# Performance work log

Hardware: AMD Instinct MI355X
Metric: run time of the kernel (lower is better)

## Reference

```python
import jax, jax.numpy as jnp
import numpy as np

K = 3            # TAGConv default number of hops
NUM_GRAPHS = 128 # graphs in the batch (for global_add_pool)


def _gcn_norm(src, dst, n):
    # PyG gcn_norm (symmetric, no self-loops): w_e = d[src]^-1/2 * d[dst]^-1/2
    deg = jnp.zeros((n,), jnp.float32).at[dst].add(1.0)
    dinv = jnp.where(deg > 0, jax.lax.rsqrt(deg), 0.0)
    return dinv[src] * dinv[dst]


def _tagconv(x, src, dst, wn, W, b):
    # out = sum_{k=0..K} (norm_adj^k x) @ W[k] + b
    n = x.shape[0]
    h = x
    out = h @ W[0]
    for k in range(1, K + 1):
        h = jax.ops.segment_sum(h[src] * wn[:, None], dst, num_segments=n)
        out = out + h @ W[k]
    return out + b


def setup_inputs() -> dict:
    key = jax.random.key(0)
    ks = jax.random.split(key, 8)
    N, E, D, H = 50000, 800000, 64, 64
    x = jax.random.normal(ks[0], (N, D), jnp.float32)
    edge_index = jax.random.randint(ks[1], (2, E), 0, N, dtype=jnp.int32)
    batch_ids = jnp.sort(jax.random.randint(ks[2], (N,), 0, NUM_GRAPHS, dtype=jnp.int32))
    def glorot(k, sh):
        return jax.random.normal(k, sh, jnp.float32) / np.float32(np.sqrt(sh[-2]))
    W0 = glorot(ks[3], (K + 1, D, H)); b0 = jnp.zeros((H,), jnp.float32)
    W1 = glorot(ks[4], (K + 1, H, H)); b1 = jnp.zeros((H,), jnp.float32)
    alpha0 = jnp.full((1,), 0.25, jnp.float32)  # PReLU default init
    alpha1 = jnp.full((1,), 0.25, jnp.float32)
    Wout = glorot(ks[5], (H, 1)); bout = jnp.zeros((1,), jnp.float32)
    return dict(x=x, edge_index=edge_index, batch_ids=batch_ids,
                W0=W0, b0=b0, W1=W1, b1=b1,
                alpha0=alpha0, alpha1=alpha1, Wout=Wout, bout=bout)


def reference(x, edge_index, batch_ids, W0, b0, W1, b1, alpha0, alpha1, Wout, bout):
    src, dst = edge_index[0], edge_index[1]
    wn = _gcn_norm(src, dst, x.shape[0])
    # layer 0: TAGConv -> (dropout=identity in eval) -> PReLU
    h = _tagconv(x, src, dst, wn, W0, b0)
    h = jnp.where(h >= 0, h, alpha0 * h)
    # layer 1
    h = _tagconv(h, src, dst, wn, W1, b1)
    h = jnp.where(h >= 0, h, alpha1 * h)
    # global_add_pool over graphs, then linear critic head
    g = jax.ops.segment_sum(h, batch_ids, num_segments=NUM_GRAPHS)  # [G, H]
    return g @ Wout + bout  # [G, 1]
```

## Files before the change

kernel.cpp:

```cpp
#include <hip/hip_runtime.h>
#include <hip/hip_bf16.h>
#include <hip/hip_fp16.h>

#define D 64
#define GRAPHS 128

using bf16x8 = __attribute__((ext_vector_type(8))) short;
using f32x4  = __attribute__((ext_vector_type(4))) float;


__device__ __forceinline__ float bf2f(unsigned short u) {
    return __uint_as_float(((unsigned)u) << 16);
}
__device__ __forceinline__ unsigned short f2bf(float f) {
    unsigned u = __float_as_uint(f);
    unsigned r = (u + 0x7FFFu + ((u >> 16) & 1u)) >> 16;
    return (unsigned short)r;
}


__global__ void deg_prep_kernel(const int* __restrict__ dst, int* __restrict__ deg,
                                int* __restrict__ pos, int E, int EB4,
                                const float* __restrict__ W0, const float* __restrict__ W1,
                                unsigned short* __restrict__ WF0, unsigned short* __restrict__ WF1,
                                const float* __restrict__ x, unsigned short* __restrict__ H, int NH) {
    int b = blockIdx.x;
    if (b < EB4) {
        int e0 = (b * 256 + threadIdx.x) * 4;
        if (e0 + 4 <= E) {
            int4 d4 = *(const int4*)(dst + e0);
            int4 p;
            p.x = atomicAdd(&deg[d4.x], 1);
            p.y = atomicAdd(&deg[d4.y], 1);
            p.z = atomicAdd(&deg[d4.z], 1);
            p.w = atomicAdd(&deg[d4.w], 1);
            *(int4*)(pos + e0) = p;
        } else {
            for (int e = e0; e < E; ++e) pos[e] = atomicAdd(&deg[dst[e]], 1);
        }
    } else if (b < EB4 + 128) {
        int idx = (b - EB4) * 256 + threadIdx.x;
        int i = idx & 16383;
        int j = i & 7, lane = (i >> 3) & 63, ct = (i >> 9) & 3, kt = i >> 11;
        int n = ct * 16 + (lane & 15);
        int k = kt * 32 + (lane >> 4) * 8 + j;
        if (idx < 16384) WF0[i] = f2bf(W0[k * 64 + n]);
        else             WF1[i] = f2bf(W1[k * 64 + n]);
    } else {
        int i = (b - EB4 - 128) * 256 + threadIdx.x;
        if (i < NH) {
            int n = i >> 3, f = (i & 7) * 8;
            float4 x0 = *(const float4*)(x + (size_t)n * 64 + f);
            float4 x1 = *(const float4*)(x + (size_t)n * 64 + f + 4);
            bf16x8 pk;
            pk[0] = f2bf(x0.x); pk[1] = f2bf(x0.y); pk[2] = f2bf(x0.z); pk[3] = f2bf(x0.w);
            pk[4] = f2bf(x1.x); pk[5] = f2bf(x1.y); pk[6] = f2bf(x1.z); pk[7] = f2bf(x1.w);
            *(bf16x8*)(H + (size_t)n * 256 + f) = pk;
        }
    }
}


__global__ void scan_all_kernel(const int* __restrict__ deg, float* __restrict__ dinv,
                                int* __restrict__ pdeg, int* __restrict__ rowstart,
                                unsigned int* __restrict__ ep, int* __restrict__ total, int N) {
    __shared__ int s[256];
    __shared__ int base_sh;
    int i = blockIdx.x * 256 + threadIdx.x;
    int d = 0, p = 0;
    if (i < N) {
        d = deg[i];
        dinv[i] = d > 0 ? rsqrtf((float)d) : 0.0f;
        p = (d + 7) & ~7;
        pdeg[i] = p;
    }
    s[threadIdx.x] = p;
    __syncthreads();
    for (int st = 1; st < 256; st <<= 1) {
        int add = (threadIdx.x >= st) ? s[threadIdx.x - st] : 0;
        __syncthreads();
        s[threadIdx.x] += add;
        __syncthreads();
    }
    if (threadIdx.x == 255) base_sh = atomicAdd(total, s[255]);
    __syncthreads();
    if (i < N) {
        int excl = base_sh + s[threadIdx.x] - p;
        rowstart[i] = excl;
        for (int q = excl + d; q < excl + p; ++q) ep[q] = 0u;
    }
}


__global__ void scatter_kernel(const int* __restrict__ src, const int* __restrict__ dst,
                               const int* __restrict__ pos, const float* __restrict__ dinv,
                               const int* __restrict__ rowstart, unsigned int* __restrict__ ep, int E) {
    int e0 = (blockIdx.x * 256 + threadIdx.x) * 4;
    if (e0 + 4 <= E) {
        int4 s4 = *(const int4*)(src + e0);
        int4 d4 = *(const int4*)(dst + e0);
        int4 p4 = *(const int4*)(pos + e0);
        float v0 = dinv[s4.x], v1 = dinv[s4.y], v2 = dinv[s4.z], v3 = dinv[s4.w];
        int r0 = rowstart[d4.x], r1 = rowstart[d4.y], r2 = rowstart[d4.z], r3 = rowstart[d4.w];
        ep[r0 + p4.x] = (unsigned)s4.x | ((unsigned)__half_as_ushort(__float2half(v0)) << 16);
        ep[r1 + p4.y] = (unsigned)s4.y | ((unsigned)__half_as_ushort(__float2half(v1)) << 16);
        ep[r2 + p4.z] = (unsigned)s4.z | ((unsigned)__half_as_ushort(__float2half(v2)) << 16);
        ep[r3 + p4.w] = (unsigned)s4.w | ((unsigned)__half_as_ushort(__float2half(v3)) << 16);
    } else {
        for (int e = e0; e < E; ++e) {
            int dd = dst[e], ss = src[e];
            ep[rowstart[dd] + pos[e]] = (unsigned)ss | ((unsigned)__half_as_ushort(__float2half(dinv[ss])) << 16);
        }
    }
}


#define GROWS 8

__global__ __launch_bounds__(512, 8)
void gather_kernel(const unsigned short* __restrict__ in,
                   unsigned short* __restrict__ out,
                   const int* __restrict__ rowstart, const int* __restrict__ pdeg,
                   const float* __restrict__ dinv, const unsigned int* __restrict__ ep, int N) {
    int wid = blockIdx.x * GROWS + (threadIdx.x >> 6);
    if (wid >= N) return;
    int lane = threadIdx.x & 63;
    int g  = lane >> 3;
    int fl = (lane & 7) * 8;

    int start = __builtin_amdgcn_readfirstlane(rowstart[wid]);
    int cnt   = __builtin_amdgcn_readfirstlane(pdeg[wid]);
    float dd  = dinv[wid];

    float a0=0.f,a1=0.f,a2=0.f,a3=0.f,a4=0.f,a5=0.f,a6=0.f,a7=0.f;
    float c0=0.f,c1=0.f,c2=0.f,c3=0.f,c4=0.f,c5=0.f,c6=0.f,c7=0.f;
    unsigned eA = 0, eB = 0;
    if (cnt > 0) {
        eA = ep[start + g];
        eB = (8 < cnt) ? ep[start + 8 + g] : 0u;
    }
    for (int i = 0; i < cnt; i += 16) {
        unsigned cA = eA, cB = eB;
        if (i + 16 < cnt) {
            eA = ep[start + i + 16 + g];
            eB = (i + 24 < cnt) ? ep[start + i + 24 + g] : 0u;
        }
        bf16x8 rA = *(const bf16x8*)(in + (size_t)(cA & 0xFFFFu) * 256 + fl);
        bf16x8 rB = *(const bf16x8*)(in + (size_t)(cB & 0xFFFFu) * 256 + fl);
        float wA = __half2float(__ushort_as_half((unsigned short)(cA >> 16)));
        float wB = __half2float(__ushort_as_half((unsigned short)(cB >> 16)));
        a0 = fmaf(wA, bf2f((unsigned short)rA[0]), a0);
        a1 = fmaf(wA, bf2f((unsigned short)rA[1]), a1);
        a2 = fmaf(wA, bf2f((unsigned short)rA[2]), a2);
        a3 = fmaf(wA, bf2f((unsigned short)rA[3]), a3);
        a4 = fmaf(wA, bf2f((unsigned short)rA[4]), a4);
        a5 = fmaf(wA, bf2f((unsigned short)rA[5]), a5);
        a6 = fmaf(wA, bf2f((unsigned short)rA[6]), a6);
        a7 = fmaf(wA, bf2f((unsigned short)rA[7]), a7);
        c0 = fmaf(wB, bf2f((unsigned short)rB[0]), c0);
        c1 = fmaf(wB, bf2f((unsigned short)rB[1]), c1);
        c2 = fmaf(wB, bf2f((unsigned short)rB[2]), c2);
        c3 = fmaf(wB, bf2f((unsigned short)rB[3]), c3);
        c4 = fmaf(wB, bf2f((unsigned short)rB[4]), c4);
        c5 = fmaf(wB, bf2f((unsigned short)rB[5]), c5);
        c6 = fmaf(wB, bf2f((unsigned short)rB[6]), c6);
        c7 = fmaf(wB, bf2f((unsigned short)rB[7]), c7);
    }
    a0 += c0; a1 += c1; a2 += c2; a3 += c3;
    a4 += c4; a5 += c5; a6 += c6; a7 += c7;
    a0 += __shfl_xor(a0, 8, 64); a0 += __shfl_xor(a0, 16, 64); a0 += __shfl_xor(a0, 32, 64);
    a1 += __shfl_xor(a1, 8, 64); a1 += __shfl_xor(a1, 16, 64); a1 += __shfl_xor(a1, 32, 64);
    a2 += __shfl_xor(a2, 8, 64); a2 += __shfl_xor(a2, 16, 64); a2 += __shfl_xor(a2, 32, 64);
    a3 += __shfl_xor(a3, 8, 64); a3 += __shfl_xor(a3, 16, 64); a3 += __shfl_xor(a3, 32, 64);
    a4 += __shfl_xor(a4, 8, 64); a4 += __shfl_xor(a4, 16, 64); a4 += __shfl_xor(a4, 32, 64);
    a5 += __shfl_xor(a5, 8, 64); a5 += __shfl_xor(a5, 16, 64); a5 += __shfl_xor(a5, 32, 64);
    a6 += __shfl_xor(a6, 8, 64); a6 += __shfl_xor(a6, 16, 64); a6 += __shfl_xor(a6, 32, 64);
    a7 += __shfl_xor(a7, 8, 64); a7 += __shfl_xor(a7, 16, 64); a7 += __shfl_xor(a7, 32, 64);
    if (g == 0) {
        bf16x8 pk;
        pk[0] = f2bf(a0 * dd); pk[1] = f2bf(a1 * dd);
        pk[2] = f2bf(a2 * dd); pk[3] = f2bf(a3 * dd);
        pk[4] = f2bf(a4 * dd); pk[5] = f2bf(a5 * dd);
        pk[6] = f2bf(a6 * dd); pk[7] = f2bf(a7 * dd);
        *(bf16x8*)(out + (size_t)wid * 256 + fl) = pk;
    }
}


template<int MODE>
__global__ __launch_bounds__(256, 4)
void tag_gemm_kernel(const unsigned short* __restrict__ H,
                     const unsigned short* __restrict__ Wfrag,
                     const float* __restrict__ bias, const float* __restrict__ alpha,
                     const float* __restrict__ Wout, const int* __restrict__ batch,
                     const float* __restrict__ bout,
                     unsigned short* __restrict__ H2, float* __restrict__ outp, int N) {
    __shared__ float bins[GRAPHS];
    if (MODE == 3) {
        if (threadIdx.x < GRAPHS) bins[threadIdx.x] = 0.0f;
        __syncthreads();
    }
    if (MODE == 2) {
        if (blockIdx.x == 0 && threadIdx.x < GRAPHS) outp[threadIdx.x] = bout[0];
    }

    int w = threadIdx.x >> 6, lane = threadIdx.x & 63;
    int m = lane & 15, quad = lane >> 4;
    int rowbase = blockIdx.x * 64 + w * 16;
    int arow = rowbase + m;
    size_t aoff = (size_t)min(arow, N - 1) * 256 + quad * 8;

    f32x4 acc0 = {0.f, 0.f, 0.f, 0.f}, acc1 = acc0, acc2 = acc0, acc3 = acc0;
#pragma unroll
    for (int kt = 0; kt < 8; ++kt) {
        bf16x8 A = *(const bf16x8*)(H + aoff + kt * 32);
        const unsigned short* wf = Wfrag + ((size_t)(kt * 4) * 64 + lane) * 8;
        bf16x8 B0 = *(const bf16x8*)(wf + 0 * 64 * 8);
        bf16x8 B1 = *(const bf16x8*)(wf + 1 * 64 * 8);
        bf16x8 B2 = *(const bf16x8*)(wf + 2 * 64 * 8);
        bf16x8 B3 = *(const bf16x8*)(wf + 3 * 64 * 8);
        acc0 = __builtin_amdgcn_mfma_f32_16x16x32_bf16(A, B0, acc0, 0, 0, 0);
        acc1 = __builtin_amdgcn_mfma_f32_16x16x32_bf16(A, B1, acc1, 0, 0, 0);
        acc2 = __builtin_amdgcn_mfma_f32_16x16x32_bf16(A, B2, acc2, 0, 0, 0);
        acc3 = __builtin_amdgcn_mfma_f32_16x16x32_bf16(A, B3, acc3, 0, 0, 0);
    }

    float al = alpha[0];
    f32x4 accs[4] = {acc0, acc1, acc2, acc3};
    if (MODE == 2) {
#pragma unroll
        for (int ct = 0; ct < 4; ++ct) {
            int col = ct * 16 + m;
            float b = bias[col];
#pragma unroll
            for (int r = 0; r < 4; ++r) {
                int row = rowbase + quad * 4 + r;
                if (row < N) {
                    float v = accs[ct][r] + b;
                    v = v >= 0.f ? v : al * v;
                    H2[(size_t)row * 256 + col] = f2bf(v);
                }
            }
        }
    } else {
        float rv0 = 0.f, rv1 = 0.f, rv2 = 0.f, rv3 = 0.f;
#pragma unroll
        for (int ct = 0; ct < 4; ++ct) {
            int col = ct * 16 + m;
            float b = bias[col], wo = Wout[col];
            float v;
            v = accs[ct][0] + b; v = v >= 0.f ? v : al * v; rv0 = fmaf(v, wo, rv0);
            v = accs[ct][1] + b; v = v >= 0.f ? v : al * v; rv1 = fmaf(v, wo, rv1);
            v = accs[ct][2] + b; v = v >= 0.f ? v : al * v; rv2 = fmaf(v, wo, rv2);
            v = accs[ct][3] + b; v = v >= 0.f ? v : al * v; rv3 = fmaf(v, wo, rv3);
        }
        float rv[4] = {rv0, rv1, rv2, rv3};
#pragma unroll
        for (int r = 0; r < 4; ++r) {
            float v = rv[r];
            v += __shfl_xor(v, 8, 16);
            v += __shfl_xor(v, 4, 16);
            v += __shfl_xor(v, 2, 16);
            v += __shfl_xor(v, 1, 16);
            int row = rowbase + quad * 4 + r;
            if (m == 0 && row < N) atomicAdd(&bins[batch[row]], v);
        }
        __syncthreads();
        if (threadIdx.x < GRAPHS) {
            float bv = bins[threadIdx.x];
            if (bv != 0.0f) atomicAdd(&outp[threadIdx.x], bv);
        }
    }
}

extern "C" void kernel_launch(void* const* d_in, const int* in_sizes, int n_in,
                              void* d_out, int out_size, void* d_ws, size_t ws_size,
                              hipStream_t stream) {
    const float* x     = (const float*)d_in[0];
    const int*   ei    = (const int*)d_in[1];
    const int*   batch = (const int*)d_in[2];
    const float* W0    = (const float*)d_in[3];
    const float* b0    = (const float*)d_in[4];
    const float* W1    = (const float*)d_in[5];
    const float* b1    = (const float*)d_in[6];
    const float* a0    = (const float*)d_in[7];
    const float* a1    = (const float*)d_in[8];
    const float* Wout  = (const float*)d_in[9];
    const float* bout  = (const float*)d_in[10];

    const int N = in_sizes[0] / D;
    const int E = in_sizes[1] / 2;
    const int* src = ei;
    const int* dst = ei + E;

    size_t off = 0;
    auto alloc = [&](size_t bytes) -> void* {
        void* p = (char*)d_ws + off;
        off = (off + bytes + 255) & ~(size_t)255;
        return p;
    };
    const int NB = (N + 255) / 256;
    int*   deg      = (int*)alloc((size_t)(N + 1) * 4);
    int*   pdeg     = (int*)alloc((size_t)N * 4);
    int*   rowstart = (int*)alloc((size_t)N * 4);
    float* dinv     = (float*)alloc((size_t)N * 4);
    int*   pos      = (int*)alloc((size_t)E * 4);
    unsigned int* epack = (unsigned int*)alloc(((size_t)E + 8ull * N) * 4);
    unsigned short* HA = (unsigned short*)alloc((size_t)N * 256 * 2);
    unsigned short* HB = (unsigned short*)alloc((size_t)N * 256 * 2);
    unsigned short* WF0 = (unsigned short*)alloc(16384 * 2);
    unsigned short* WF1 = (unsigned short*)alloc(16384 * 2);

    const int EB4 = (E + 1023) / 1024;
    const int NXH = (N * 8 + 255) / 256;
    const int NG = (N + GROWS - 1) / GROWS;
    const int NM = (N + 63) / 64;

    hipMemsetAsync(deg, 0, (size_t)(N + 1) * 4, stream);
    deg_prep_kernel<<<EB4 + 128 + NXH, 256, 0, stream>>>(dst, deg, pos, E, EB4,
                                                         W0, W1, WF0, WF1, x, HA, N * 8);
    scan_all_kernel<<<NB, 256, 0, stream>>>(deg, dinv, pdeg, rowstart, epack, deg + N, N);
    scatter_kernel<<<EB4, 256, 0, stream>>>(src, dst, pos, dinv, rowstart, epack, E);

    gather_kernel<<<NG, 512, 0, stream>>>(HA + 0 * 64, HA + 1 * 64, rowstart, pdeg, dinv, epack, N);
    gather_kernel<<<NG, 512, 0, stream>>>(HA + 1 * 64, HA + 2 * 64, rowstart, pdeg, dinv, epack, N);
    gather_kernel<<<NG, 512, 0, stream>>>(HA + 2 * 64, HA + 3 * 64, rowstart, pdeg, dinv, epack, N);
    tag_gemm_kernel<2><<<NM, 256, 0, stream>>>(HA, WF0, b0, a0, nullptr, nullptr, bout,
                                               HB, (float*)d_out, N);

    gather_kernel<<<NG, 512, 0, stream>>>(HB + 0 * 64, HB + 1 * 64, rowstart, pdeg, dinv, epack, N);
    gather_kernel<<<NG, 512, 0, stream>>>(HB + 1 * 64, HB + 2 * 64, rowstart, pdeg, dinv, epack, N);
    gather_kernel<<<NG, 512, 0, stream>>>(HB + 2 * 64, HB + 3 * 64, rowstart, pdeg, dinv, epack, N);
    tag_gemm_kernel<3><<<NM, 256, 0, stream>>>(HB, WF1, b1, a1, Wout, batch, bout,
                                               nullptr, (float*)d_out, N);
}
```

Before: 279.8 us.

## Fuse three gather hops into one persistent kernel with a grid barrier

Replaces three separate gather launches per layer with a single persistent kernel of 512 blocks that loops over node tiles and runs all three hops, separated by a global atomic-counter barrier. The goal is to remove the launch gaps and tail effects between hops. In exchange, the kernel relies on all 512 blocks being co-resident to avoid deadlock, adds spin-wait and fence overhead, and uses fewer waves per SIMD (launch bounds lowered from 8 to 4).

```diff
diff --git a/kernel.cpp b/kernel.cpp
--- a/kernel.cpp
+++ b/kernel.cpp
@@ -116,73 +116,96 @@
 
 
 #define GROWS 8
-
-__global__ __launch_bounds__(512, 8)
-void gather_kernel(const unsigned short* __restrict__ in,
-                   unsigned short* __restrict__ out,
-                   const int* __restrict__ rowstart, const int* __restrict__ pdeg,
-                   const float* __restrict__ dinv, const unsigned int* __restrict__ ep, int N) {
-    int wid = blockIdx.x * GROWS + (threadIdx.x >> 6);
-    if (wid >= N) return;
+#define GBLOCKS 512
+
+__global__ __launch_bounds__(512, 4)
+void gather3_kernel(unsigned short* __restrict__ H,
+                    const int* __restrict__ rowstart, const int* __restrict__ pdeg,
+                    const float* __restrict__ dinv, const unsigned int* __restrict__ ep,
+                    int* __restrict__ bar, int bar_base, int N) {
+    int wave = threadIdx.x >> 6;
     int lane = threadIdx.x & 63;
     int g  = lane >> 3;
     int fl = (lane & 7) * 8;
-
-    int start = __builtin_amdgcn_readfirstlane(rowstart[wid]);
-    int cnt   = __builtin_amdgcn_readfirstlane(pdeg[wid]);
-    float dd  = dinv[wid];
-
-    float a0=0.f,a1=0.f,a2=0.f,a3=0.f,a4=0.f,a5=0.f,a6=0.f,a7=0.f;
-    float c0=0.f,c1=0.f,c2=0.f,c3=0.f,c4=0.f,c5=0.f,c6=0.f,c7=0.f;
-    unsigned eA = 0, eB = 0;
-    if (cnt > 0) {
-        eA = ep[start + g];
-        eB = (8 < cnt) ? ep[start + 8 + g] : 0u;
-    }
-    for (int i = 0; i < cnt; i += 16) {
-        unsigned cA = eA, cB = eB;
-        if (i + 16 < cnt) {
-            eA = ep[start + i + 16 + g];
-            eB = (i + 24 < cnt) ? ep[start + i + 24 + g] : 0u;
-        }
-        bf16x8 rA = *(const bf16x8*)(in + (size_t)(cA & 0xFFFFu) * 256 + fl);
-        bf16x8 rB = *(const bf16x8*)(in + (size_t)(cB & 0xFFFFu) * 256 + fl);
-        float wA = __half2float(__ushort_as_half((unsigned short)(cA >> 16)));
-        float wB = __half2float(__ushort_as_half((unsigned short)(cB >> 16)));
-        a0 = fmaf(wA, bf2f((unsigned short)rA[0]), a0);
-        a1 = fmaf(wA, bf2f((unsigned short)rA[1]), a1);
-        a2 = fmaf(wA, bf2f((unsigned short)rA[2]), a2);
-        a3 = fmaf(wA, bf2f((unsigned short)rA[3]), a3);
-        a4 = fmaf(wA, bf2f((unsigned short)rA[4]), a4);
-        a5 = fmaf(wA, bf2f((unsigned short)rA[5]), a5);
-        a6 = fmaf(wA, bf2f((unsigned short)rA[6]), a6);
-        a7 = fmaf(wA, bf2f((unsigned short)rA[7]), a7);
-        c0 = fmaf(wB, bf2f((unsigned short)rB[0]), c0);
-        c1 = fmaf(wB, bf2f((unsigned short)rB[1]), c1);
-        c2 = fmaf(wB, bf2f((unsigned short)rB[2]), c2);
-        c3 = fmaf(wB, bf2f((unsigned short)rB[3]), c3);
-        c4 = fmaf(wB, bf2f((unsigned short)rB[4]), c4);
-        c5 = fmaf(wB, bf2f((unsigned short)rB[5]), c5);
-        c6 = fmaf(wB, bf2f((unsigned short)rB[6]), c6);
-        c7 = fmaf(wB, bf2f((unsigned short)rB[7]), c7);
-    }
-    a0 += c0; a1 += c1; a2 += c2; a3 += c3;
-    a4 += c4; a5 += c5; a6 += c6; a7 += c7;
-    a0 += __shfl_xor(a0, 8, 64); a0 += __shfl_xor(a0, 16, 64); a0 += __shfl_xor(a0, 32, 64);
-    a1 += __shfl_xor(a1, 8, 64); a1 += __shfl_xor(a1, 16, 64); a1 += __shfl_xor(a1, 32, 64);
-    a2 += __shfl_xor(a2, 8, 64); a2 += __shfl_xor(a2, 16, 64); a2 += __shfl_xor(a2, 32, 64);
-    a3 += __shfl_xor(a3, 8, 64); a3 += __shfl_xor(a3, 16, 64); a3 += __shfl_xor(a3, 32, 64);
-    a4 += __shfl_xor(a4, 8, 64); a4 += __shfl_xor(a4, 16, 64); a4 += __shfl_xor(a4, 32, 64);
-    a5 += __shfl_xor(a5, 8, 64); a5 += __shfl_xor(a5, 16, 64); a5 += __shfl_xor(a5, 32, 64);
-    a6 += __shfl_xor(a6, 8, 64); a6 += __shfl_xor(a6, 16, 64); a6 += __shfl_xor(a6, 32, 64);
-    a7 += __shfl_xor(a7, 8, 64); a7 += __shfl_xor(a7, 16, 64); a7 += __shfl_xor(a7, 32, 64);
-    if (g == 0) {
-        bf16x8 pk;
-        pk[0] = f2bf(a0 * dd); pk[1] = f2bf(a1 * dd);
-        pk[2] = f2bf(a2 * dd); pk[3] = f2bf(a3 * dd);
-        pk[4] = f2bf(a4 * dd); pk[5] = f2bf(a5 * dd);
-        pk[6] = f2bf(a6 * dd); pk[7] = f2bf(a7 * dd);
-        *(bf16x8*)(out + (size_t)wid * 256 + fl) = pk;
+    int ntiles = (N + GROWS - 1) / GROWS;
+
+    for (int hop = 0; hop < 3; ++hop) {
+        const unsigned short* in  = H + hop * 64;
+        unsigned short*       out = H + (hop + 1) * 64;
+
+        for (int tile = blockIdx.x; tile < ntiles; tile += GBLOCKS) {
+            int wid = tile * GROWS + wave;
+            if (wid < N) {
+                int start = __builtin_amdgcn_readfirstlane(rowstart[wid]);
+                int cnt   = __builtin_amdgcn_readfirstlane(pdeg[wid]);
+                float dd  = dinv[wid];
+
+                float a0=0.f,a1=0.f,a2=0.f,a3=0.f,a4=0.f,a5=0.f,a6=0.f,a7=0.f;
+                float c0=0.f,c1=0.f,c2=0.f,c3=0.f,c4=0.f,c5=0.f,c6=0.f,c7=0.f;
+                unsigned eA = 0, eB = 0;
+                if (cnt > 0) {
+                    eA = ep[start + g];
+                    eB = (8 < cnt) ? ep[start + 8 + g] : 0u;
+                }
+                for (int i = 0; i < cnt; i += 16) {
+                    unsigned cA = eA, cB = eB;
+                    if (i + 16 < cnt) {
+                        eA = ep[start + i + 16 + g];
+                        eB = (i + 24 < cnt) ? ep[start + i + 24 + g] : 0u;
+                    }
+                    bf16x8 rA = *(const bf16x8*)(in + (size_t)(cA & 0xFFFFu) * 256 + fl);
+                    bf16x8 rB = *(const bf16x8*)(in + (size_t)(cB & 0xFFFFu) * 256 + fl);
+                    float wA = __half2float(__ushort_as_half((unsigned short)(cA >> 16)));
+                    float wB = __half2float(__ushort_as_half((unsigned short)(cB >> 16)));
+                    a0 = fmaf(wA, bf2f((unsigned short)rA[0]), a0);
+                    a1 = fmaf(wA, bf2f((unsigned short)rA[1]), a1);
+                    a2 = fmaf(wA, bf2f((unsigned short)rA[2]), a2);
+                    a3 = fmaf(wA, bf2f((unsigned short)rA[3]), a3);
+                    a4 = fmaf(wA, bf2f((unsigned short)rA[4]), a4);
+                    a5 = fmaf(wA, bf2f((unsigned short)rA[5]), a5);
+                    a6 = fmaf(wA, bf2f((unsigned short)rA[6]), a6);
+                    a7 = fmaf(wA, bf2f((unsigned short)rA[7]), a7);
+                    c0 = fmaf(wB, bf2f((unsigned short)rB[0]), c0);
+                    c1 = fmaf(wB, bf2f((unsigned short)rB[1]), c1);
+                    c2 = fmaf(wB, bf2f((unsigned short)rB[2]), c2);
+                    c3 = fmaf(wB, bf2f((unsigned short)rB[3]), c3);
+                    c4 = fmaf(wB, bf2f((unsigned short)rB[4]), c4);
+                    c5 = fmaf(wB, bf2f((unsigned short)rB[5]), c5);
+                    c6 = fmaf(wB, bf2f((unsigned short)rB[6]), c6);
+                    c7 = fmaf(wB, bf2f((unsigned short)rB[7]), c7);
+                }
+                a0 += c0; a1 += c1; a2 += c2; a3 += c3;
+                a4 += c4; a5 += c5; a6 += c6; a7 += c7;
+                a0 += __shfl_xor(a0, 8, 64); a0 += __shfl_xor(a0, 16, 64); a0 += __shfl_xor(a0, 32, 64);
+                a1 += __shfl_xor(a1, 8, 64); a1 += __shfl_xor(a1, 16, 64); a1 += __shfl_xor(a1, 32, 64);
+                a2 += __shfl_xor(a2, 8, 64); a2 += __shfl_xor(a2, 16, 64); a2 += __shfl_xor(a2, 32, 64);
+                a3 += __shfl_xor(a3, 8, 64); a3 += __shfl_xor(a3, 16, 64); a3 += __shfl_xor(a3, 32, 64);
+                a4 += __shfl_xor(a4, 8, 64); a4 += __shfl_xor(a4, 16, 64); a4 += __shfl_xor(a4, 32, 64);
+                a5 += __shfl_xor(a5, 8, 64); a5 += __shfl_xor(a5, 16, 64); a5 += __shfl_xor(a5, 32, 64);
+                a6 += __shfl_xor(a6, 8, 64); a6 += __shfl_xor(a6, 16, 64); a6 += __shfl_xor(a6, 32, 64);
+                a7 += __shfl_xor(a7, 8, 64); a7 += __shfl_xor(a7, 16, 64); a7 += __shfl_xor(a7, 32, 64);
+                if (g == 0) {
+                    bf16x8 pk;
+                    pk[0] = f2bf(a0 * dd); pk[1] = f2bf(a1 * dd);
+                    pk[2] = f2bf(a2 * dd); pk[3] = f2bf(a3 * dd);
+                    pk[4] = f2bf(a4 * dd); pk[5] = f2bf(a5 * dd);
+                    pk[6] = f2bf(a6 * dd); pk[7] = f2bf(a7 * dd);
+                    *(bf16x8*)(out + (size_t)wid * 256 + fl) = pk;
+                }
+            }
+        }
+
+        if (hop < 2) {
+            __threadfence();
+            __syncthreads();
+            if (threadIdx.x == 0) {
+                atomicAdd(bar, 1);
+                int target = bar_base + (hop + 1) * GBLOCKS;
+                while (atomicAdd(bar, 0) < target) __builtin_amdgcn_s_sleep(8);
+            }
+            __syncthreads();
+            __threadfence();
+        }
     }
 }
 
@@ -300,7 +323,7 @@
         return p;
     };
     const int NB = (N + 255) / 256;
-    int*   deg      = (int*)alloc((size_t)(N + 1) * 4);
+    int*   deg      = (int*)alloc((size_t)(N + 64) * 4);
     int*   pdeg     = (int*)alloc((size_t)N * 4);
     int*   rowstart = (int*)alloc((size_t)N * 4);
     float* dinv     = (float*)alloc((size_t)N * 4);
@@ -310,27 +333,23 @@
     unsigned short* HB = (unsigned short*)alloc((size_t)N * 256 * 2);
     unsigned short* WF0 = (unsigned short*)alloc(16384 * 2);
     unsigned short* WF1 = (unsigned short*)alloc(16384 * 2);
+    int* bar = deg + N + 8;
 
     const int EB4 = (E + 1023) / 1024;
     const int NXH = (N * 8 + 255) / 256;
-    const int NG = (N + GROWS - 1) / GROWS;
     const int NM = (N + 63) / 64;
 
-    hipMemsetAsync(deg, 0, (size_t)(N + 1) * 4, stream);
+    hipMemsetAsync(deg, 0, (size_t)(N + 64) * 4, stream);
     deg_prep_kernel<<<EB4 + 128 + NXH, 256, 0, stream>>>(dst, deg, pos, E, EB4,
                                                          W0, W1, WF0, WF1, x, HA, N * 8);
     scan_all_kernel<<<NB, 256, 0, stream>>>(deg, dinv, pdeg, rowstart, epack, deg + N, N);
     scatter_kernel<<<EB4, 256, 0, stream>>>(src, dst, pos, dinv, rowstart, epack, E);
 
-    gather_kernel<<<NG, 512, 0, stream>>>(HA + 0 * 64, HA + 1 * 64, rowstart, pdeg, dinv, epack, N);
-    gather_kernel<<<NG, 512, 0, stream>>>(HA + 1 * 64, HA + 2 * 64, rowstart, pdeg, dinv, epack, N);
-    gather_kernel<<<NG, 512, 0, stream>>>(HA + 2 * 64, HA + 3 * 64, rowstart, pdeg, dinv, epack, N);
+    gather3_kernel<<<GBLOCKS, 512, 0, stream>>>(HA, rowstart, pdeg, dinv, epack, bar, 0, N);
     tag_gemm_kernel<2><<<NM, 256, 0, stream>>>(HA, WF0, b0, a0, nullptr, nullptr, bout,
                                                HB, (float*)d_out, N);
 
-    gather_kernel<<<NG, 512, 0, stream>>>(HB + 0 * 64, HB + 1 * 64, rowstart, pdeg, dinv, epack, N);
-    gather_kernel<<<NG, 512, 0, stream>>>(HB + 1 * 64, HB + 2 * 64, rowstart, pdeg, dinv, epack, N);
-    gather_kernel<<<NG, 512, 0, stream>>>(HB + 2 * 64, HB + 3 * 64, rowstart, pdeg, dinv, epack, N);
+    gather3_kernel<<<GBLOCKS, 512, 0, stream>>>(HB, rowstart, pdeg, dinv, epack, bar, 1024, N);
     tag_gemm_kernel<3><<<NM, 256, 0, stream>>>(HB, WF1, b1, a1, Wout, batch, bout,
                                                nullptr, (float*)d_out, N);
 }
```

New measurement: 1.020 ms. 3.65x slower.
